# Optimization experiments

Measured on AMD Instinct MI355X. Metric: run time of the kernel, lower is better.

Reference implementation:

```python
import jax, jax.numpy as jnp
import numpy as np

N = 262144          # active voxels
C_IN = 64
C_OUT = 64
BATCH = 2
D0, D1, D2 = 128, 128, 128   # sparse spatial grid
VOL = D0 * D1 * D2


def setup_inputs() -> dict:
    key = jax.random.key(0)
    kf, kw = jax.random.split(key, 2)
    # unique voxel coordinates (submanifold conv assumes no duplicate sites)
    rng = np.random.default_rng(0)
    packed = rng.choice(BATCH * VOL, size=N, replace=False)
    b = packed // VOL
    r = packed % VOL
    i0 = r // (D1 * D2)
    r2 = r % (D1 * D2)
    i1 = r2 // D2
    i2 = r2 % D2
    indices = jnp.asarray(np.stack([b, i0, i1, i2], axis=1), dtype=jnp.int32)  # [N,4]
    features = jax.random.normal(kf, (N, C_IN), dtype=jnp.float32)
    # KRSC layout: [out_ch, k0, k1, k2, in_ch], trunc_normal(std=0.02) ~ normal here
    weight = jax.random.normal(kw, (C_OUT, 3, 3, 3, C_IN), dtype=jnp.float32) * 0.02
    bias = jnp.zeros((C_OUT,), dtype=jnp.float32)
    return {"features": features, "weight": weight, "bias": bias, "indices": indices}


def reference(features, weight, bias, indices):
    n = features.shape[0]
    idx = indices.astype(jnp.int32)
    # linearize (b, i0, i1, i2); packing is linear in coords so neighbor pack = pack + shift
    packed = idx[:, 0] * VOL + idx[:, 1] * (D1 * D2) + idx[:, 2] * D2 + idx[:, 3]
    order = jnp.argsort(packed)
    sorted_pack = packed[order]
    out = jnp.zeros((n, C_OUT), dtype=features.dtype)
    for k0 in range(3):
        for k1 in range(3):
            for k2 in range(3):
                shift = (k0 - 1) * (D1 * D2) + (k1 - 1) * D2 + (k2 - 1)
                neigh_pack = packed + shift
                p = jnp.searchsorted(sorted_pack, neigh_pack)
                pc = jnp.minimum(p, n - 1)
                ok = (p < n) & (sorted_pack[pc] == neigh_pack)
                src = jnp.where(ok, order[pc], 0)
                gathered = jnp.where(ok[:, None], features[src], 0.0)  # [N, C_in]
                out = out + gathered @ weight[:, k0, k1, k2, :].T      # [N, C_out]
    return out + bias
```

## Files before the change

### kernel.cpp

```cpp
#include <hip/hip_runtime.h>

#define VOL   2097152
#define TBL   4194304
#define D1D2  16384
#define DD2   128

typedef __bf16 bf16_t;
typedef bf16_t bf16x4 __attribute__((ext_vector_type(4)));
typedef bf16_t bf16x8 __attribute__((ext_vector_type(8)));
typedef float  floatx4 __attribute__((ext_vector_type(4)));


__global__ void build_table_k(const int* __restrict__ idx, int* __restrict__ table, int n) {
    int t = blockIdx.x * blockDim.x + threadIdx.x;
    if (t < n) {
        int4 c = ((const int4*)idx)[t];
        int p = ((c.x * 128 + c.y) * 128 + c.z) * 128 + c.w;
        table[p] = t;
    }
}

__global__ void cvt_feat_k(const float* __restrict__ f, bf16_t* __restrict__ fb, int n4) {
    int t = blockIdx.x * blockDim.x + threadIdx.x;
    if (t < n4) {
        float4 v = ((const float4*)f)[t];
        bf16x4 o = { (bf16_t)v.x, (bf16_t)v.y, (bf16_t)v.z, (bf16_t)v.w };
        ((bf16x4*)fb)[t] = o;
    }
}

__global__ void cvt_w_k(const float* __restrict__ w, bf16_t* __restrict__ wb) {
    int t = blockIdx.x * blockDim.x + threadIdx.x;
    if (t < 27 * 64 * 64) {
        int ci = t & 63;
        int co = (t >> 6) & 63;
        int k  = t >> 12;
        wb[t] = (bf16_t)w[(co * 27 + k) * 64 + ci];
    }
}


__global__ __launch_bounds__(256) void conv_k(
        const bf16_t* __restrict__ fb, const bf16_t* __restrict__ wb,
        const int* __restrict__ table, const int* __restrict__ idx,
        const float* __restrict__ bias, float* __restrict__ out, int n)
{
    __shared__ int    s_packed[64];
    __shared__ bf16_t sF[64 * 72];
    __shared__ bf16_t sW[64 * 72];

    const int t    = threadIdx.x;
    const int tile = blockIdx.x * 64;

    if (t < 64) {
        int vn = tile + t;
        if (vn < n) {
            int4 c = ((const int4*)idx)[vn];
            s_packed[t] = ((c.x * 128 + c.y) * 128 + c.z) * 128 + c.w;
        } else {
            s_packed[t] = (int)0xC0000000;
        }
    }

    const int lane = t & 63;
    const int w    = t >> 6;
    const int l15  = lane & 15;
    const int q    = lane >> 4;
    const int r    = t >> 2;
    const int j    = t & 3;

    floatx4 acc[4] = { {0,0,0,0}, {0,0,0,0}, {0,0,0,0}, {0,0,0,0} };

    __syncthreads();
    const int pk = s_packed[r];

    for (int k = 0; k < 27; ++k) {
        int k0 = k / 9, k1 = (k / 3) % 3, k2 = k % 3;
        int shift = (k0 - 1) * D1D2 + (k1 - 1) * DD2 + (k2 - 1);

        __syncthreads();

        int np  = pk + shift;
        int nbr = (np >= 0 && np < TBL) ? table[np] : -1;
        bf16x8 v0 = {}, v1 = {};
        if (nbr >= 0) {
            const bf16x8* src = (const bf16x8*)(fb + nbr * 64 + j * 16);
            v0 = src[0];
            v1 = src[1];
        }
        *(bf16x8*)&sF[r * 72 + j * 16]     = v0;
        *(bf16x8*)&sF[r * 72 + j * 16 + 8] = v1;

        {
            const bf16x8* wsrc = (const bf16x8*)(wb + (k * 64 + r) * 64 + j * 16);
            *(bf16x8*)&sW[r * 72 + j * 16]     = wsrc[0];
            *(bf16x8*)&sW[r * 72 + j * 16 + 8] = wsrc[1];
        }

        __syncthreads();

        #pragma unroll
        for (int s = 0; s < 2; ++s) {
            bf16x8 a = *(const bf16x8*)&sW[(w * 16 + l15) * 72 + s * 32 + q * 8];
            #pragma unroll
            for (int g = 0; g < 4; ++g) {
                bf16x8 b = *(const bf16x8*)&sF[(g * 16 + l15) * 72 + s * 32 + q * 8];
                acc[g] = __builtin_amdgcn_mfma_f32_16x16x32_bf16(a, b, acc[g], 0, 0, 0);
            }
        }
    }

    float4 bs = *(const float4*)&bias[w * 16 + q * 4];
    #pragma unroll
    for (int g = 0; g < 4; ++g) {
        int vn = tile + g * 16 + l15;
        if (vn < n) {
            float4 o;
            o.x = acc[g][0] + bs.x;
            o.y = acc[g][1] + bs.y;
            o.z = acc[g][2] + bs.z;
            o.w = acc[g][3] + bs.w;
            *(float4*)&out[vn * 64 + w * 16 + q * 4] = o;
        }
    }
}


extern "C" void kernel_launch(void* const* d_in, const int* in_sizes, int n_in,
                              void* d_out, int out_size, void* d_ws, size_t ws_size,
                              hipStream_t stream) {
    const float* feat = (const float*)d_in[0];
    const float* wgt  = (const float*)d_in[1];
    const float* bias = (const float*)d_in[2];
    const int*   idx  = (const int*)d_in[3];
    float* out = (float*)d_out;

    const int n = in_sizes[0] / 64;

    char* ws = (char*)d_ws;
    int*    table = (int*)ws;
    bf16_t* wbf   = (bf16_t*)(ws + (size_t)TBL * 4);
    bf16_t* fbf   = (bf16_t*)(ws + (size_t)TBL * 4 + 262144);

    hipMemsetAsync(table, 0xFF, (size_t)TBL * 4, stream);
    build_table_k<<<(n + 255) / 256, 256, 0, stream>>>(idx, table, n);

    int n4 = n * 16;
    cvt_feat_k<<<(n4 + 255) / 256, 256, 0, stream>>>(feat, fbf, n4);
    cvt_w_k<<<(27 * 4096 + 255) / 256, 256, 0, stream>>>(wgt, wbf);

    int blocks = (n + 63) / 64;
    conv_k<<<blocks, 256, 0, stream>>>(fbf, wbf, table, idx, bias, out, n);
}
```

Measured before the change: 240.2 us.

## Fuse prep kernels, double tile size, precompute neighbors, register-prefetch next offset

```diff
diff --git a/kernel.cpp b/kernel.cpp
--- a/kernel.cpp
+++ b/kernel.cpp
@@ -4,38 +4,45 @@
 #define TBL   4194304
 #define D1D2  16384
 #define DD2   128
+#define TILE  128
 
 typedef __bf16 bf16_t;
-typedef bf16_t bf16x4 __attribute__((ext_vector_type(4)));
 typedef bf16_t bf16x8 __attribute__((ext_vector_type(8)));
 typedef float  floatx4 __attribute__((ext_vector_type(4)));
 
 
-__global__ void build_table_k(const int* __restrict__ idx, int* __restrict__ table, int n) {
-    int t = blockIdx.x * blockDim.x + threadIdx.x;
-    if (t < n) {
-        int4 c = ((const int4*)idx)[t];
-        int p = ((c.x * 128 + c.y) * 128 + c.z) * 128 + c.w;
-        table[p] = t;
-    }
-}
-
-__global__ void cvt_feat_k(const float* __restrict__ f, bf16_t* __restrict__ fb, int n4) {
-    int t = blockIdx.x * blockDim.x + threadIdx.x;
-    if (t < n4) {
-        float4 v = ((const float4*)f)[t];
-        bf16x4 o = { (bf16_t)v.x, (bf16_t)v.y, (bf16_t)v.z, (bf16_t)v.w };
-        ((bf16x4*)fb)[t] = o;
-    }
-}
-
-__global__ void cvt_w_k(const float* __restrict__ w, bf16_t* __restrict__ wb) {
-    int t = blockIdx.x * blockDim.x + threadIdx.x;
-    if (t < 27 * 64 * 64) {
-        int ci = t & 63;
-        int co = (t >> 6) & 63;
-        int k  = t >> 12;
-        wb[t] = (bf16_t)w[(co * 27 + k) * 64 + ci];
+__global__ __launch_bounds__(256) void prep_k(const float* __restrict__ f,
+                                              const float* __restrict__ w,
+                                              const int* __restrict__ idx,
+                                              int* __restrict__ table,
+                                              bf16_t* __restrict__ wb,
+                                              bf16_t* __restrict__ fb, int n) {
+    const int b = blockIdx.x;
+    const int tblB = (n + 255) >> 8;
+    if (b < tblB) {
+        int t = b * 256 + threadIdx.x;
+        if (t < n) {
+            int4 c = ((const int4*)idx)[t];
+            int p = ((c.x * 128 + c.y) * 128 + c.z) * 128 + c.w;
+            table[p] = t;
+        }
+    } else if (b < tblB + 432) {
+        int t = (b - tblB) * 256 + threadIdx.x;
+        if (t < 27 * 64 * 64) {
+            int ci = t & 63, co = (t >> 6) & 63, k = t >> 12;
+            wb[t] = (bf16_t)w[(co * 27 + k) * 64 + ci];
+        }
+    } else {
+        int t = (b - tblB - 432) * 256 + threadIdx.x;
+        int pos = t >> 3, c = (t & 7) * 8;
+        if (pos < n) {
+            const float* src = f + (size_t)pos * 64 + c;
+            float4 a  = *(const float4*)src;
+            float4 b2 = *(const float4*)(src + 4);
+            bf16x8 o = { (bf16_t)a.x,  (bf16_t)a.y,  (bf16_t)a.z,  (bf16_t)a.w,
+                         (bf16_t)b2.x, (bf16_t)b2.y, (bf16_t)b2.z, (bf16_t)b2.w };
+            *(bf16x8*)(fb + (size_t)pos * 64 + c) = o;
+        }
     }
 }
 
@@ -45,56 +52,88 @@
         const int* __restrict__ table, const int* __restrict__ idx,
         const float* __restrict__ bias, float* __restrict__ out, int n)
 {
-    __shared__ int    s_packed[64];
-    __shared__ bf16_t sF[64 * 72];
+    __shared__ int    s_pkd[TILE];
+    __shared__ int    s_nbr[27 * TILE];
+    __shared__ bf16_t sF[TILE * 72];
     __shared__ bf16_t sW[64 * 72];
 
     const int t    = threadIdx.x;
-    const int tile = blockIdx.x * 64;
+    const int tile = blockIdx.x * TILE;
 
-    if (t < 64) {
+    if (t < TILE) {
         int vn = tile + t;
         if (vn < n) {
             int4 c = ((const int4*)idx)[vn];
-            s_packed[t] = ((c.x * 128 + c.y) * 128 + c.z) * 128 + c.w;
+            s_pkd[t] = ((c.x * 128 + c.y) * 128 + c.z) * 128 + c.w;
         } else {
-            s_packed[t] = (int)0xC0000000;
+            s_pkd[t] = (int)0xC0000000;
         }
+    }
+    __syncthreads();
+
+    for (int u = t; u < 27 * TILE; u += 256) {
+        int k  = u >> 7;
+        int r  = u & (TILE - 1);
+        int k0 = k / 9, k1 = (k / 3) % 3, k2 = k % 3;
+        int np = s_pkd[r] + (k0 - 1) * D1D2 + (k1 - 1) * DD2 + (k2 - 1);
+        s_nbr[u] = (np >= 0 && np < TBL) ? table[np] : -1;
     }
 
     const int lane = t & 63;
     const int w    = t >> 6;
     const int l15  = lane & 15;
     const int q    = lane >> 4;
-    const int r    = t >> 2;
-    const int j    = t & 3;
 
-    floatx4 acc[4] = { {0,0,0,0}, {0,0,0,0}, {0,0,0,0}, {0,0,0,0} };
+    const int rF = t >> 1;
+    const int hF = t & 1;
+    const int rW = t >> 2;
+    const int cW = t & 3;
+
+    floatx4 acc[8] = {};
 
     __syncthreads();
-    const int pk = s_packed[r];
+
+    bf16x8 pf[4] = {{}, {}, {}, {}};
+    bf16x8 pw0, pw1;
+    {
+        int nbr = s_nbr[rF];
+        if (nbr >= 0) {
+            const bf16x8* src = (const bf16x8*)(fb + (size_t)nbr * 64 + hF * 32);
+            pf[0] = src[0];
+            pf[1] = src[1];
+            pf[2] = src[2];
+            pf[3] = src[3];
+        }
+        const bf16x8* wsrc = (const bf16x8*)(wb + rW * 64 + cW * 16);
+        pw0 = wsrc[0];
+        pw1 = wsrc[1];
+    }
 
     for (int k = 0; k < 27; ++k) {
-        int k0 = k / 9, k1 = (k / 3) % 3, k2 = k % 3;
-        int shift = (k0 - 1) * D1D2 + (k1 - 1) * DD2 + (k2 - 1);
+        *(bf16x8*)&sF[rF * 72 + hF * 32]      = pf[0];
+        *(bf16x8*)&sF[rF * 72 + hF * 32 + 8]  = pf[1];
+        *(bf16x8*)&sF[rF * 72 + hF * 32 + 16] = pf[2];
+        *(bf16x8*)&sF[rF * 72 + hF * 32 + 24] = pf[3];
+        *(bf16x8*)&sW[rW * 72 + cW * 16]      = pw0;
+        *(bf16x8*)&sW[rW * 72 + cW * 16 + 8]  = pw1;
 
-        __syncthreads();
-
-        int np  = pk + shift;
-        int nbr = (np >= 0 && np < TBL) ? table[np] : -1;
-        bf16x8 v0 = {}, v1 = {};
-        if (nbr >= 0) {
-            const bf16x8* src = (const bf16x8*)(fb + nbr * 64 + j * 16);
-            v0 = src[0];
-            v1 = src[1];
-        }
-        *(bf16x8*)&sF[r * 72 + j * 16]     = v0;
-        *(bf16x8*)&sF[r * 72 + j * 16 + 8] = v1;
-
-        {
-            const bf16x8* wsrc = (const bf16x8*)(wb + (k * 64 + r) * 64 + j * 16);
-            *(bf16x8*)&sW[r * 72 + j * 16]     = wsrc[0];
-            *(bf16x8*)&sW[r * 72 + j * 16 + 8] = wsrc[1];
+        if (k + 1 < 27) {
+            int nbr = s_nbr[(k + 1) * TILE + rF];
+            bf16x8 n0 = {}, n1 = {}, n2 = {}, n3 = {};
+            if (nbr >= 0) {
+                const bf16x8* src = (const bf16x8*)(fb + (size_t)nbr * 64 + hF * 32);
+                n0 = src[0];
+                n1 = src[1];
+                n2 = src[2];
+                n3 = src[3];
+            }
+            const bf16x8* wsrc = (const bf16x8*)(wb + ((k + 1) * 64 + rW) * 64 + cW * 16);
+            pw0   = wsrc[0];
+            pw1   = wsrc[1];
+            pf[0] = n0;
+            pf[1] = n1;
+            pf[2] = n2;
+            pf[3] = n3;
         }
 
         __syncthreads();
@@ -103,16 +142,18 @@
         for (int s = 0; s < 2; ++s) {
             bf16x8 a = *(const bf16x8*)&sW[(w * 16 + l15) * 72 + s * 32 + q * 8];
             #pragma unroll
-            for (int g = 0; g < 4; ++g) {
-                bf16x8 b = *(const bf16x8*)&sF[(g * 16 + l15) * 72 + s * 32 + q * 8];
-                acc[g] = __builtin_amdgcn_mfma_f32_16x16x32_bf16(a, b, acc[g], 0, 0, 0);
+            for (int g = 0; g < 8; ++g) {
+                bf16x8 bfrag = *(const bf16x8*)&sF[(g * 16 + l15) * 72 + s * 32 + q * 8];
+                acc[g] = __builtin_amdgcn_mfma_f32_16x16x32_bf16(a, bfrag, acc[g], 0, 0, 0);
             }
         }
+
+        __syncthreads();
     }
 
     float4 bs = *(const float4*)&bias[w * 16 + q * 4];
     #pragma unroll
-    for (int g = 0; g < 4; ++g) {
+    for (int g = 0; g < 8; ++g) {
         int vn = tile + g * 16 + l15;
         if (vn < n) {
             float4 o;
@@ -120,7 +161,7 @@
             o.y = acc[g][1] + bs.y;
             o.z = acc[g][2] + bs.z;
             o.w = acc[g][3] + bs.w;
-            *(float4*)&out[vn * 64 + w * 16 + q * 4] = o;
+            *(float4*)&out[(size_t)vn * 64 + w * 16 + q * 4] = o;
         }
     }
 }
@@ -143,12 +184,10 @@
     bf16_t* fbf   = (bf16_t*)(ws + (size_t)TBL * 4 + 262144);
 
     hipMemsetAsync(table, 0xFF, (size_t)TBL * 4, stream);
-    build_table_k<<<(n + 255) / 256, 256, 0, stream>>>(idx, table, n);
 
-    int n4 = n * 16;
-    cvt_feat_k<<<(n4 + 255) / 256, 256, 0, stream>>>(feat, fbf, n4);
-    cvt_w_k<<<(27 * 4096 + 255) / 256, 256, 0, stream>>>(wgt, wbf);
+    int tblB = (n + 255) >> 8;
+    int fB   = (n * 8 + 255) >> 8;
+    prep_k<<<tblB + 432 + fB, 256, 0, stream>>>(feat, wgt, idx, table, wbf, fbf, n);
 
-    int blocks = (n + 63) / 64;
-    conv_k<<<blocks, 256, 0, stream>>>(fbf, wbf, table, idx, bias, out, n);
+    conv_k<<<(n + TILE - 1) / TILE, 256, 0, stream>>>(fbf, wbf, table, idx, bias, out, n);
 }
```

New measurement: 239.0 us. Within noise of the previous version (-0.5%).
